# Kernel optimization log

Measured on AMD Instinct MI355X. Metric: run time of the kernel, lower is better.

## Reference

```python
import jax, jax.numpy as jnp
import numpy as np


def setup_inputs() -> dict:
    key = jax.random.key(0)
    k1, k2, k3 = jax.random.split(key, 3)
    S, G, B, C, P = 3, 8, 2048, 512, 64
    node_feats = jax.random.normal(k1, (S, G * B, C), dtype=jnp.float32)
    weight = jax.random.normal(k2, (P, C), dtype=jnp.float32)
    smooth_factor = jax.random.normal(k3, (P,), dtype=jnp.float32)
    return {
        "node_feats": node_feats,
        "weight": weight,
        "smooth_factor": smooth_factor,
        "batch_size": B,
        "num_graphs": G,
    }


def reference(node_feats, weight, smooth_factor, batch_size, num_graphs):
    # node_feats: [S, N_scale, C] (scales stacked; torch version takes a list and cats)
    S, Ns, C = node_feats.shape
    P = weight.shape[0]
    x = node_feats.reshape(-1, C)                       # [N, C], N = S*Ns

    # RBF-style score: (2*c.x - |x|^2 - |c|^2), clamped at 0, scaled by beta
    cx = x @ weight.T                                   # [N, P]
    x_sq = jnp.sum(x * x, axis=1, keepdims=True)        # [N, 1]
    c_sq = jnp.sum(weight * weight, axis=1)[None, :]    # [1, P]
    beta = jax.nn.sigmoid(smooth_factor)                # [P]
    logits = jnp.minimum(2.0 * cx - x_sq - c_sq, 0.0) / beta[None, :]
    assign = jax.nn.softmax(logits, axis=1)             # [N, P]

    # Per-graph weighted sum (uniform batch_list), accumulated across scales:
    # out[g] = sum_{s,n in graph g} assign[s,g,n]^T feats[s,g,n]
    a = assign.reshape(S, num_graphs, batch_size, P)
    f = node_feats.reshape(S, num_graphs, batch_size, C)
    outputs = jnp.einsum('sgnp,sgnc->gpc', a, f)        # [G, P, C]
    return outputs, assign
```

## Files before the change

### kernel.cpp

```cpp
#include <hip/hip_runtime.h>
#include <math.h>

#define S_ 3
#define G_ 8
#define B_ 2048
#define C_ 512
#define P_ 64
#define N_ (S_ * G_ * B_)

typedef __attribute__((ext_vector_type(8))) short short8;
typedef __attribute__((ext_vector_type(4))) short short4v;
typedef __attribute__((ext_vector_type(4))) float f32x4;

__device__ __forceinline__ unsigned short f2bf(float f) {
    union { float f; unsigned u; } c; c.f = f;
    unsigned u = c.u;
    u += 0x7fffu + ((u >> 16) & 1u);
    return (unsigned short)(u >> 16);
}

__global__ void zero_kernel(float* __restrict__ out, int n) {
    int i = blockIdx.x * blockDim.x + threadIdx.x;
    if (i < n) out[i] = 0.0f;
}

__global__ __launch_bounds__(256) void assign_mfma(
    const float* __restrict__ x,
    const float* __restrict__ w,
    const float* __restrict__ sf,
    float* __restrict__ assign)
{
    __shared__ __align__(16) short xs[64 * 72];
    __shared__ __align__(16) short ws[64 * 72];
    __shared__ float xsqp[64][16];
    __shared__ float csqp[64][16];
    __shared__ float xsq_s[64], csq_s[64], rbeta_s[64];

    const int t    = threadIdx.x;
    const int n0   = blockIdx.x * 64;
    const int lane = t & 63;
    const int wv   = t >> 6;
    const int q    = lane >> 4;
    const int col  = lane & 15;
    const int srow = t >> 4;
    const int scol = (t & 15) * 4;

    if (t < 64) rbeta_s[t] = 1.0f + expf(-sf[t]);

    f32x4 acc[4];
#pragma unroll
    for (int i = 0; i < 4; ++i) acc[i] = (f32x4){0.f, 0.f, 0.f, 0.f};

    float xacc[4] = {0.f, 0.f, 0.f, 0.f};
    float wacc[4] = {0.f, 0.f, 0.f, 0.f};

    for (int ch = 0; ch < 8; ++ch) {
        const int k0 = ch * 64;
#pragma unroll
        for (int i = 0; i < 4; ++i) {
            int row = srow + 16 * i;
            f32x4 xv = *(const f32x4*)(x + (size_t)(n0 + row) * C_ + k0 + scol);
            xacc[i] += xv.x * xv.x + xv.y * xv.y + xv.z * xv.z + xv.w * xv.w;
            short4v xb = {(short)f2bf(xv.x), (short)f2bf(xv.y),
                          (short)f2bf(xv.z), (short)f2bf(xv.w)};
            *(short4v*)&xs[row * 72 + scol] = xb;

            f32x4 wl = *(const f32x4*)(w + (size_t)row * C_ + k0 + scol);
            wacc[i] += wl.x * wl.x + wl.y * wl.y + wl.z * wl.z + wl.w * wl.w;
            short4v wb = {(short)f2bf(wl.x), (short)f2bf(wl.y),
                          (short)f2bf(wl.z), (short)f2bf(wl.w)};
            *(short4v*)&ws[row * 72 + scol] = wb;
        }
        __syncthreads();

#pragma unroll
        for (int stp = 0; stp < 2; ++stp) {
            int kb = stp * 32 + q * 8;
            short8 af = *(const short8*)&xs[(16 * wv + col) * 72 + kb];
#pragma unroll
            for (int t4 = 0; t4 < 4; ++t4) {
                short8 bf = *(const short8*)&ws[(16 * t4 + col) * 72 + kb];
                acc[t4] = __builtin_amdgcn_mfma_f32_16x16x32_bf16(af, bf, acc[t4], 0, 0, 0);
            }
        }
        __syncthreads();
    }

#pragma unroll
    for (int i = 0; i < 4; ++i) {
        xsqp[srow + 16 * i][t & 15] = xacc[i];
        csqp[srow + 16 * i][t & 15] = wacc[i];
    }
    __syncthreads();
    if (t < 64) {
        float s = 0.f;
#pragma unroll
        for (int j = 0; j < 16; ++j) s += xsqp[t][j];
        xsq_s[t] = s;
    } else if (t < 128) {
        int r = t - 64;
        float s = 0.f;
#pragma unroll
        for (int j = 0; j < 16; ++j) s += csqp[r][j];
        csq_s[r] = s;
    }
    __syncthreads();

#pragma unroll
    for (int reg = 0; reg < 4; ++reg) {
        int row = 16 * wv + 4 * q + reg;
        float vv[4];
        float vmax = -3.4e38f;
#pragma unroll
        for (int t4 = 0; t4 < 4; ++t4) {
            int p = 16 * t4 + col;
            float v = 2.0f * acc[t4][reg] - xsq_s[row] - csq_s[p];
            v = fminf(v, 0.0f) * rbeta_s[p];
            vv[t4] = v;
            vmax = fmaxf(vmax, v);
        }
#pragma unroll
        for (int off = 1; off < 16; off <<= 1)
            vmax = fmaxf(vmax, __shfl_xor(vmax, off, 64));
        float e[4], ssum = 0.f;
#pragma unroll
        for (int t4 = 0; t4 < 4; ++t4) { e[t4] = __expf(vv[t4] - vmax); ssum += e[t4]; }
#pragma unroll
        for (int off = 1; off < 16; off <<= 1)
            ssum += __shfl_xor(ssum, off, 64);
        float inv = 1.0f / ssum;
#pragma unroll
        for (int t4 = 0; t4 < 4; ++t4)
            assign[(size_t)(n0 + row) * P_ + 16 * t4 + col] = e[t4] * inv;
    }
}

__global__ __launch_bounds__(256) void group_mfma(
    const float* __restrict__ x,
    const float* __restrict__ assign,
    float* __restrict__ out)
{
    __shared__ __align__(16) short as_[64 * 66];
    __shared__ __align__(16) short fs_[64 * 66];

    const int t    = threadIdx.x;
    const int g    = blockIdx.x;
    const int c0   = blockIdx.y * 64;
    const int kc   = blockIdx.z;
    const int sc   = kc >> 2;
    const int b0   = (kc & 3) * 512;
    const int lane = t & 63;
    const int wv   = t >> 6;
    const int q    = lane >> 4;
    const int col  = lane & 15;
    const int srow = t >> 4;
    const int scol = (t & 15) * 4;

    const size_t base = (size_t)sc * (G_ * B_) + (size_t)g * B_ + b0;

    f32x4 acc[4];
#pragma unroll
    for (int i = 0; i < 4; ++i) acc[i] = (f32x4){0.f, 0.f, 0.f, 0.f};

    for (int ch = 0; ch < 8; ++ch) {
#pragma unroll
        for (int i = 0; i < 4; ++i) {
            int n = srow + 16 * i;
            size_t nn = base + ch * 64 + n;
            f32x4 av = *(const f32x4*)(assign + nn * P_ + scol);
            unsigned a01 = (unsigned)f2bf(av.x) | ((unsigned)f2bf(av.y) << 16);
            unsigned a23 = (unsigned)f2bf(av.z) | ((unsigned)f2bf(av.w) << 16);
            *(unsigned*)&as_[n * 66 + scol]     = a01;
            *(unsigned*)&as_[n * 66 + scol + 2] = a23;

            f32x4 fv = *(const f32x4*)(x + nn * C_ + c0 + scol);
            unsigned f01 = (unsigned)f2bf(fv.x) | ((unsigned)f2bf(fv.y) << 16);
            unsigned f23 = (unsigned)f2bf(fv.z) | ((unsigned)f2bf(fv.w) << 16);
            *(unsigned*)&fs_[n * 66 + scol]     = f01;
            *(unsigned*)&fs_[n * 66 + scol + 2] = f23;
        }
        __syncthreads();

#pragma unroll
        for (int stp = 0; stp < 2; ++stp) {
            int kb = stp * 32 + q * 8;
            short8 af;
#pragma unroll
            for (int j = 0; j < 8; ++j) af[j] = as_[(kb + j) * 66 + 16 * wv + col];
#pragma unroll
            for (int t4 = 0; t4 < 4; ++t4) {
                short8 bf;
#pragma unroll
                for (int j = 0; j < 8; ++j) bf[j] = fs_[(kb + j) * 66 + 16 * t4 + col];
                acc[t4] = __builtin_amdgcn_mfma_f32_16x16x32_bf16(af, bf, acc[t4], 0, 0, 0);
            }
        }
        __syncthreads();
    }

#pragma unroll
    for (int t4 = 0; t4 < 4; ++t4) {
#pragma unroll
        for (int reg = 0; reg < 4; ++reg) {
            int p = 16 * wv + 4 * q + reg;
            int c = c0 + 16 * t4 + col;
            atomicAdd(&out[(size_t)g * (P_ * C_) + (size_t)p * C_ + c], acc[t4][reg]);
        }
    }
}

extern "C" void kernel_launch(void* const* d_in, const int* in_sizes, int n_in,
                              void* d_out, int out_size, void* d_ws, size_t ws_size,
                              hipStream_t stream) {
    const float* x  = (const float*)d_in[0];
    const float* w  = (const float*)d_in[1];
    const float* sf = (const float*)d_in[2];

    float* out    = (float*)d_out;
    float* assign = out + (size_t)G_ * P_ * C_;

    zero_kernel<<<(G_ * P_ * C_ + 255) / 256, 256, 0, stream>>>(out, G_ * P_ * C_);

    assign_mfma<<<N_ / 64, 256, 0, stream>>>(x, w, sf, assign);

    dim3 gridB(G_, C_ / 64, 12);
    group_mfma<<<gridB, 256, 0, stream>>>(x, assign, out);
}
```

Measured before the change: 199.1 us.

## Precompute bf16 weights, emit transposed bf16 assign, drop LDS staging in assign kernel

A prep kernel converts the weights to bf16 once and computes the center norms and inverse betas into workspace. The assign kernel now loads x straight into MFMA fragments without LDS or block barriers, and writes an extra transposed bf16 copy of the assignments. The grouping kernel reads that transposed copy directly as its A operand and stages only the features in an XOR-swizzled LDS layout, replacing the old scalar strided LDS gathers. This adds a workspace write pass and an extra kernel launch in exchange for cheaper operand loads in both GEMMs.

```diff
diff --git a/kernel.cpp b/kernel.cpp
--- a/kernel.cpp
+++ b/kernel.cpp
@@ -9,189 +9,197 @@
 #define N_ (S_ * G_ * B_)
 
 typedef __attribute__((ext_vector_type(8))) short short8;
-typedef __attribute__((ext_vector_type(4))) short short4v;
 typedef __attribute__((ext_vector_type(4))) float f32x4;
-
-__device__ __forceinline__ unsigned short f2bf(float f) {
+typedef __attribute__((ext_vector_type(4))) unsigned int uint4v;
+typedef __attribute__((ext_vector_type(2))) unsigned int uint2v;
+
+__device__ __forceinline__ unsigned f2bf1(float f) {
     union { float f; unsigned u; } c; c.f = f;
     unsigned u = c.u;
     u += 0x7fffu + ((u >> 16) & 1u);
-    return (unsigned short)(u >> 16);
-}
-
-__global__ void zero_kernel(float* __restrict__ out, int n) {
+    return u >> 16;
+}
+__device__ __forceinline__ unsigned pk2(float a, float b) {
+    return f2bf1(a) | (f2bf1(b) << 16);
+}
+
+__global__ void zero_kernel(float* __restrict__ out) {
     int i = blockIdx.x * blockDim.x + threadIdx.x;
-    if (i < n) out[i] = 0.0f;
-}
-
-__global__ __launch_bounds__(256) void assign_mfma(
-    const float* __restrict__ x,
-    const float* __restrict__ w,
-    const float* __restrict__ sf,
-    float* __restrict__ assign)
+    ((f32x4*)out)[i] = (f32x4){0.f, 0.f, 0.f, 0.f};
+}
+
+__global__ __launch_bounds__(64) void prep_kernel(
+    const float* __restrict__ w, const float* __restrict__ sf,
+    unsigned short* __restrict__ wb, float* __restrict__ csq,
+    float* __restrict__ rbeta)
 {
-    __shared__ __align__(16) short xs[64 * 72];
-    __shared__ __align__(16) short ws[64 * 72];
-    __shared__ float xsqp[64][16];
-    __shared__ float csqp[64][16];
-    __shared__ float xsq_s[64], csq_s[64], rbeta_s[64];
+    const int p = blockIdx.x, l = threadIdx.x;
+    const float* wr = w + (size_t)p * C_ + l * 8;
+    f32x4 a = *(const f32x4*)wr;
+    f32x4 b = *(const f32x4*)(wr + 4);
+    float s = a[0]*a[0] + a[1]*a[1] + a[2]*a[2] + a[3]*a[3]
+            + b[0]*b[0] + b[1]*b[1] + b[2]*b[2] + b[3]*b[3];
+    uint4v pk;
+    pk.x = pk2(a[0], a[1]); pk.y = pk2(a[2], a[3]);
+    pk.z = pk2(b[0], b[1]); pk.w = pk2(b[2], b[3]);
+    *(uint4v*)&wb[(size_t)p * C_ + l * 8] = pk;
+#pragma unroll
+    for (int off = 1; off < 64; off <<= 1) s += __shfl_xor(s, off, 64);
+    if (l == 0) csq[p] = s;
+    if (p == 0) rbeta[l] = 1.0f + expf(-sf[l]);
+}
+
+__global__ __launch_bounds__(256) void assign_v2(
+    const float* __restrict__ x, const unsigned short* __restrict__ wb,
+    const float* __restrict__ csq, const float* __restrict__ rbeta,
+    float* __restrict__ assign, unsigned short* __restrict__ a_t)
+{
+    __shared__ float lg[64 * 68];
 
     const int t    = threadIdx.x;
-    const int n0   = blockIdx.x * 64;
     const int lane = t & 63;
     const int wv   = t >> 6;
     const int q    = lane >> 4;
     const int col  = lane & 15;
-    const int srow = t >> 4;
-    const int scol = (t & 15) * 4;
-
-    if (t < 64) rbeta_s[t] = 1.0f + expf(-sf[t]);
+    const int n0   = blockIdx.x * 64;
+    const int myrow = 16 * wv + col;
+
+    const float* xr = x + (size_t)(n0 + myrow) * C_ + q * 8;
+
+    float csqv[4], rbv[4];
+#pragma unroll
+    for (int t4 = 0; t4 < 4; ++t4) {
+        csqv[t4] = csq[16 * t4 + col];
+        rbv[t4]  = rbeta[16 * t4 + col];
+    }
 
     f32x4 acc[4];
 #pragma unroll
     for (int i = 0; i < 4; ++i) acc[i] = (f32x4){0.f, 0.f, 0.f, 0.f};
-
-    float xacc[4] = {0.f, 0.f, 0.f, 0.f};
-    float wacc[4] = {0.f, 0.f, 0.f, 0.f};
-
-    for (int ch = 0; ch < 8; ++ch) {
-        const int k0 = ch * 64;
-#pragma unroll
-        for (int i = 0; i < 4; ++i) {
-            int row = srow + 16 * i;
-            f32x4 xv = *(const f32x4*)(x + (size_t)(n0 + row) * C_ + k0 + scol);
-            xacc[i] += xv.x * xv.x + xv.y * xv.y + xv.z * xv.z + xv.w * xv.w;
-            short4v xb = {(short)f2bf(xv.x), (short)f2bf(xv.y),
-                          (short)f2bf(xv.z), (short)f2bf(xv.w)};
-            *(short4v*)&xs[row * 72 + scol] = xb;
-
-            f32x4 wl = *(const f32x4*)(w + (size_t)row * C_ + k0 + scol);
-            wacc[i] += wl.x * wl.x + wl.y * wl.y + wl.z * wl.z + wl.w * wl.w;
-            short4v wb = {(short)f2bf(wl.x), (short)f2bf(wl.y),
-                          (short)f2bf(wl.z), (short)f2bf(wl.w)};
-            *(short4v*)&ws[row * 72 + scol] = wb;
-        }
-        __syncthreads();
-
-#pragma unroll
-        for (int stp = 0; stp < 2; ++stp) {
-            int kb = stp * 32 + q * 8;
-            short8 af = *(const short8*)&xs[(16 * wv + col) * 72 + kb];
-#pragma unroll
-            for (int t4 = 0; t4 < 4; ++t4) {
-                short8 bf = *(const short8*)&ws[(16 * t4 + col) * 72 + kb];
-                acc[t4] = __builtin_amdgcn_mfma_f32_16x16x32_bf16(af, bf, acc[t4], 0, 0, 0);
-            }
-        }
-        __syncthreads();
-    }
-
-#pragma unroll
-    for (int i = 0; i < 4; ++i) {
-        xsqp[srow + 16 * i][t & 15] = xacc[i];
-        csqp[srow + 16 * i][t & 15] = wacc[i];
-    }
-    __syncthreads();
-    if (t < 64) {
-        float s = 0.f;
-#pragma unroll
-        for (int j = 0; j < 16; ++j) s += xsqp[t][j];
-        xsq_s[t] = s;
-    } else if (t < 128) {
-        int r = t - 64;
-        float s = 0.f;
-#pragma unroll
-        for (int j = 0; j < 16; ++j) s += csqp[r][j];
-        csq_s[r] = s;
-    }
-    __syncthreads();
+    float xsq = 0.f;
+
+#pragma unroll
+    for (int ks = 0; ks < 16; ++ks) {
+        f32x4 a = *(const f32x4*)(xr + ks * 32);
+        f32x4 b = *(const f32x4*)(xr + ks * 32 + 4);
+        xsq += a[0]*a[0] + a[1]*a[1] + a[2]*a[2] + a[3]*a[3]
+             + b[0]*b[0] + b[1]*b[1] + b[2]*b[2] + b[3]*b[3];
+        union { uint4v u; short8 s; } cvt;
+        cvt.u.x = pk2(a[0], a[1]); cvt.u.y = pk2(a[2], a[3]);
+        cvt.u.z = pk2(b[0], b[1]); cvt.u.w = pk2(b[2], b[3]);
+        short8 af = cvt.s;
+#pragma unroll
+        for (int t4 = 0; t4 < 4; ++t4) {
+            short8 bf = *(const short8*)&wb[(size_t)(16 * t4 + col) * C_ + ks * 32 + q * 8];
+            acc[t4] = __builtin_amdgcn_mfma_f32_16x16x32_bf16(af, bf, acc[t4], 0, 0, 0);
+        }
+    }
+
+    xsq += __shfl_xor(xsq, 16, 64);
+    xsq += __shfl_xor(xsq, 32, 64);
+    float xsqr[4];
+#pragma unroll
+    for (int reg = 0; reg < 4; ++reg) xsqr[reg] = __shfl(xsq, 4 * q + reg, 64);
 
 #pragma unroll
     for (int reg = 0; reg < 4; ++reg) {
-        int row = 16 * wv + 4 * q + reg;
-        float vv[4];
-        float vmax = -3.4e38f;
+        const int row = 16 * wv + 4 * q + reg;
+        float vv[4], vmax = -3.4e38f;
 #pragma unroll
         for (int t4 = 0; t4 < 4; ++t4) {
-            int p = 16 * t4 + col;
-            float v = 2.0f * acc[t4][reg] - xsq_s[row] - csq_s[p];
-            v = fminf(v, 0.0f) * rbeta_s[p];
+            float v = 2.0f * acc[t4][reg] - xsqr[reg] - csqv[t4];
+            v = fminf(v, 0.0f) * rbv[t4];
             vv[t4] = v;
             vmax = fmaxf(vmax, v);
         }
 #pragma unroll
         for (int off = 1; off < 16; off <<= 1)
             vmax = fmaxf(vmax, __shfl_xor(vmax, off, 64));
-        float e[4], ssum = 0.f;
-#pragma unroll
-        for (int t4 = 0; t4 < 4; ++t4) { e[t4] = __expf(vv[t4] - vmax); ssum += e[t4]; }
+        float e[4], ss = 0.f;
+#pragma unroll
+        for (int t4 = 0; t4 < 4; ++t4) { e[t4] = __expf(vv[t4] - vmax); ss += e[t4]; }
 #pragma unroll
         for (int off = 1; off < 16; off <<= 1)
-            ssum += __shfl_xor(ssum, off, 64);
-        float inv = 1.0f / ssum;
-#pragma unroll
-        for (int t4 = 0; t4 < 4; ++t4)
-            assign[(size_t)(n0 + row) * P_ + 16 * t4 + col] = e[t4] * inv;
-    }
-}
-
-__global__ __launch_bounds__(256) void group_mfma(
-    const float* __restrict__ x,
-    const float* __restrict__ assign,
+            ss += __shfl_xor(ss, off, 64);
+        const float inv = 1.0f / ss;
+#pragma unroll
+        for (int t4 = 0; t4 < 4; ++t4) {
+            const float val = e[t4] * inv;
+            assign[(size_t)(n0 + row) * P_ + 16 * t4 + col] = val;
+            lg[row * 68 + 16 * t4 + col] = val;
+        }
+    }
+    __syncthreads();
+
+    const int p  = t >> 2;
+    const int nq = t & 3;
+    float v[16];
+#pragma unroll
+    for (int i = 0; i < 16; ++i) v[i] = lg[(nq * 16 + i) * 68 + p];
+    uint4v d0, d1;
+    d0.x = pk2(v[0], v[1]);  d0.y = pk2(v[2], v[3]);
+    d0.z = pk2(v[4], v[5]);  d0.w = pk2(v[6], v[7]);
+    d1.x = pk2(v[8], v[9]);  d1.y = pk2(v[10], v[11]);
+    d1.z = pk2(v[12], v[13]); d1.w = pk2(v[14], v[15]);
+    unsigned short* dst = a_t + (size_t)p * N_ + n0 + nq * 16;
+    *(uint4v*)dst = d0;
+    *(uint4v*)(dst + 8) = d1;
+}
+
+__global__ __launch_bounds__(256) void group_v3(
+    const float* __restrict__ x, const unsigned short* __restrict__ a_t,
     float* __restrict__ out)
 {
-    __shared__ __align__(16) short as_[64 * 66];
-    __shared__ __align__(16) short fs_[64 * 66];
+    __shared__ unsigned int fsu[64 * 36];
 
     const int t    = threadIdx.x;
+    const int lane = t & 63;
+    const int wv   = t >> 6;
+    const int q    = lane >> 4;
+    const int col  = lane & 15;
     const int g    = blockIdx.x;
     const int c0   = blockIdx.y * 64;
     const int kc   = blockIdx.z;
     const int sc   = kc >> 2;
     const int b0   = (kc & 3) * 512;
-    const int lane = t & 63;
-    const int wv   = t >> 6;
-    const int q    = lane >> 4;
-    const int col  = lane & 15;
     const int srow = t >> 4;
-    const int scol = (t & 15) * 4;
+    const int scol = t & 15;
 
     const size_t base = (size_t)sc * (G_ * B_) + (size_t)g * B_ + b0;
+    const unsigned short* at_row = a_t + (size_t)(16 * wv + col) * N_ + base;
 
     f32x4 acc[4];
 #pragma unroll
     for (int i = 0; i < 4; ++i) acc[i] = (f32x4){0.f, 0.f, 0.f, 0.f};
 
     for (int ch = 0; ch < 8; ++ch) {
-#pragma unroll
-        for (int i = 0; i < 4; ++i) {
-            int n = srow + 16 * i;
-            size_t nn = base + ch * 64 + n;
-            f32x4 av = *(const f32x4*)(assign + nn * P_ + scol);
-            unsigned a01 = (unsigned)f2bf(av.x) | ((unsigned)f2bf(av.y) << 16);
-            unsigned a23 = (unsigned)f2bf(av.z) | ((unsigned)f2bf(av.w) << 16);
-            *(unsigned*)&as_[n * 66 + scol]     = a01;
-            *(unsigned*)&as_[n * 66 + scol + 2] = a23;
-
-            f32x4 fv = *(const f32x4*)(x + nn * C_ + c0 + scol);
-            unsigned f01 = (unsigned)f2bf(fv.x) | ((unsigned)f2bf(fv.y) << 16);
-            unsigned f23 = (unsigned)f2bf(fv.z) | ((unsigned)f2bf(fv.w) << 16);
-            *(unsigned*)&fs_[n * 66 + scol]     = f01;
-            *(unsigned*)&fs_[n * 66 + scol + 2] = f23;
+        const int nb = ch * 64;
+        const size_t rbase = (base + nb + srow * 4) * C_ + c0 + scol * 4;
+        f32x4 m0 = *(const f32x4*)(x + rbase);
+        f32x4 m1 = *(const f32x4*)(x + rbase + C_);
+        f32x4 m2 = *(const f32x4*)(x + rbase + 2 * C_);
+        f32x4 m3 = *(const f32x4*)(x + rbase + 3 * C_);
+        const int sw_w = (scol & 6) << 3;
+        const int nsw  = (srow * 4) ^ sw_w;
+#pragma unroll
+        for (int cc = 0; cc < 4; ++cc) {
+            uint2v u;
+            u.x = pk2(m0[cc], m1[cc]);
+            u.y = pk2(m2[cc], m3[cc]);
+            const int cl = scol * 4 + cc;
+            *(uint2v*)&fsu[cl * 36 + (nsw >> 1)] = u;
         }
         __syncthreads();
 
 #pragma unroll
         for (int stp = 0; stp < 2; ++stp) {
-            int kb = stp * 32 + q * 8;
-            short8 af;
-#pragma unroll
-            for (int j = 0; j < 8; ++j) af[j] = as_[(kb + j) * 66 + 16 * wv + col];
+            const int kb = stp * 32 + q * 8;
+            short8 af = *(const short8*)(at_row + nb + kb);
 #pragma unroll
             for (int t4 = 0; t4 < 4; ++t4) {
-                short8 bf;
-#pragma unroll
-                for (int j = 0; j < 8; ++j) bf[j] = fs_[(kb + j) * 66 + 16 * t4 + col];
+                const int c  = 16 * t4 + col;
+                const int sw = ((c >> 2) & 6) << 3;
+                short8 bf = *(const short8*)&fsu[c * 36 + ((kb ^ sw) >> 1)];
                 acc[t4] = __builtin_amdgcn_mfma_f32_16x16x32_bf16(af, bf, acc[t4], 0, 0, 0);
             }
         }
@@ -202,8 +210,8 @@
     for (int t4 = 0; t4 < 4; ++t4) {
 #pragma unroll
         for (int reg = 0; reg < 4; ++reg) {
-            int p = 16 * wv + 4 * q + reg;
-            int c = c0 + 16 * t4 + col;
+            const int p = 16 * wv + 4 * q + reg;
+            const int c = c0 + 16 * t4 + col;
             atomicAdd(&out[(size_t)g * (P_ * C_) + (size_t)p * C_ + c], acc[t4][reg]);
         }
     }
@@ -219,10 +227,14 @@
     float* out    = (float*)d_out;
     float* assign = out + (size_t)G_ * P_ * C_;
 
-    zero_kernel<<<(G_ * P_ * C_ + 255) / 256, 256, 0, stream>>>(out, G_ * P_ * C_);
-
-    assign_mfma<<<N_ / 64, 256, 0, stream>>>(x, w, sf, assign);
-
+    unsigned short* wb    = (unsigned short*)d_ws;
+    float*          csq   = (float*)((char*)d_ws + 65536);
+    float*          rbeta = (float*)((char*)d_ws + 65792);
+    unsigned short* a_t   = (unsigned short*)((char*)d_ws + 66048);
+
+    zero_kernel<<<(G_ * P_ * C_) / (4 * 256), 256, 0, stream>>>(out);
+    prep_kernel<<<P_, 64, 0, stream>>>(w, sf, wb, csq, rbeta);
+    assign_v2<<<N_ / 64, 256, 0, stream>>>(x, wb, csq, rbeta, assign, a_t);
     dim3 gridB(G_, C_ / 64, 12);
-    group_mfma<<<gridB, 256, 0, stream>>>(x, assign, out);
-}
+    group_v3<<<gridB, 256, 0, stream>>>(x, a_t, out);
+}
```

Result: faster. 194.3 us (-2.4%).
